# Kernel tuning notes

Hardware: AMD Instinct MI355X
Metric: run time of the kernel (lower is better)

Reference implementation:

```python
import jax, jax.numpy as jnp
import numpy as np

N_NODES = 50000
N_EDGES = 400000
LATENT = 128
HIDDEN = 512
N_HEADS = 2          # latent // 64, NodeAttn default num_heads
HEAD_DIM = LATENT // N_HEADS
N_GRAPHS = 500
LN_EPS = 1e-5


def setup_inputs() -> dict:
    key = jax.random.key(0)
    ks = jax.random.split(key, 24)
    s = 0.02
    inp = {
        "edges": jax.random.randint(ks[0], (2, N_EDGES), 0, N_NODES, dtype=jnp.int32),
        "node_feat": jax.random.normal(ks[1], (N_NODES, LATENT), jnp.float32),
        "edge_attr": jax.random.normal(ks[2], (N_EDGES, LATENT), jnp.float32),
        "u": jax.random.normal(ks[3], (N_GRAPHS, LATENT), jnp.float32),
        "num_nodes": jnp.full((N_GRAPHS,), N_NODES // N_GRAPHS, jnp.int32),
        # NodeAttn params (shared for sent/received calls, as in the module)
        "w1": jax.random.normal(ks[4], (3 * LATENT, LATENT), jnp.float32) * s,
        "b1": jnp.zeros((LATENT,), jnp.float32),
        "w2": jax.random.normal(ks[5], (N_HEADS, HEAD_DIM), jnp.float32) * s,
        "w3": jax.random.normal(ks[6], (2 * LATENT, LATENT), jnp.float32) * s,
        "b3": jnp.zeros((LATENT,), jnp.float32),
        # Encoder MLP: 4*latent -> hidden -> hidden -> latent, LN before ReLU
        "mw0": jax.random.normal(ks[7], (4 * LATENT, HIDDEN), jnp.float32) * s,
        "mb0": jnp.zeros((HIDDEN,), jnp.float32),
        "ls0": jnp.ones((HIDDEN,), jnp.float32),
        "lb0": jnp.zeros((HIDDEN,), jnp.float32),
        "mw1": jax.random.normal(ks[8], (HIDDEN, HIDDEN), jnp.float32) * s,
        "mb1": jnp.zeros((HIDDEN,), jnp.float32),
        "ls1": jnp.ones((HIDDEN,), jnp.float32),
        "lb1": jnp.zeros((HIDDEN,), jnp.float32),
        "mw2": jax.random.normal(ks[9], (HIDDEN, LATENT), jnp.float32) * s,
        "mb2": jnp.zeros((LATENT,), jnp.float32),
    }
    return inp


def _layer_norm(x, scale, bias):
    mu = jnp.mean(x, axis=-1, keepdims=True)
    var = jnp.mean(jnp.square(x - mu), axis=-1, keepdims=True)
    return (x - mu) * jax.lax.rsqrt(var + LN_EPS) * scale + bias


def _node_attn(q, k, ea, index, n_nodes, w1, b1, w2, w3, b3):
    # per-edge multi-head scores -> segment softmax over destination index -> scatter-add
    h = jax.nn.leaky_relu(jnp.concatenate([q, k, ea], axis=-1) @ w1 + b1, 0.2)
    h = h.reshape(-1, N_HEADS, HEAD_DIM)                    # [E, H, D]
    logits = jnp.einsum("ehd,hd->eh", h, w2)                 # [E, H]
    m = jax.ops.segment_max(logits, index, num_segments=n_nodes)
    m = jnp.where(jnp.isfinite(m), m, 0.0)                   # empty segments
    e = jnp.exp(logits - m[index])
    z = jax.ops.segment_sum(e, index, num_segments=n_nodes)
    alpha = e / (z[index] + 1e-16)                           # [E, H]
    v = (jnp.concatenate([k, ea], axis=-1) @ w3 + b3).reshape(-1, N_HEADS, HEAD_DIM)
    out = jax.ops.segment_sum(alpha[..., None] * v, index, num_segments=n_nodes)
    return out.reshape(n_nodes, LATENT)


def reference(edges, node_feat, edge_attr, u, num_nodes, w1, b1, w2, w3, b3,
              mw0, mb0, ls0, lb0, mw1, mb1, ls1, lb1, mw2, mb2):
    n = node_feat.shape[0]
    row, col = edges[0], edges[1]
    sent = _node_attn(node_feat[row], node_feat[col], edge_attr, row, n, w1, b1, w2, w3, b3)
    recv = _node_attn(node_feat[col], node_feat[row], edge_attr, col, n, w1, b1, w2, w3, b3)
    glob = jnp.repeat(u, num_nodes, axis=0, total_repeat_length=n)
    x = jnp.concatenate([node_feat, sent, recv, glob], axis=1)   # [N, 4*latent]
    h = jax.nn.relu(_layer_norm(x @ mw0 + mb0, ls0, lb0))
    h = jax.nn.relu(_layer_norm(h @ mw1 + mb1, ls1, lb1))
    return h @ mw2 + mb2
```

## Files before the change

### kernel.cpp

```cpp
#include <hip/hip_runtime.h>
#include <math.h>

#define LATENT 128

typedef __attribute__((ext_vector_type(8))) short bf16x8;
typedef __attribute__((ext_vector_type(4))) float f32x4;
typedef __attribute__((ext_vector_type(2))) float f32x2;
typedef __attribute__((ext_vector_type(2))) int i32x2;
typedef __attribute__((ext_vector_type(2))) unsigned u32x2;
typedef __attribute__((ext_vector_type(4))) unsigned u32x4;

union U4B { uint4 u; bf16x8 v; };

template <typename T>
__device__ __forceinline__ T ntl(const T* p) { return __builtin_nontemporal_load(p); }

__device__ __forceinline__ unsigned short f2bf(float f) {
    unsigned int x = __float_as_uint(f);
    unsigned int r = (x + 0x7fffu + ((x >> 16) & 1u)) >> 16;
    return (unsigned short)r;
}
__device__ __forceinline__ float bf2f(unsigned short h) {
    return __uint_as_float(((unsigned int)h) << 16);
}
__device__ __forceinline__ unsigned pk2(float a, float b) {
    return (unsigned)f2bf(a) | ((unsigned)f2bf(b) << 16);
}

__device__ __forceinline__ void gld16(const void* g, void* l) {
    __builtin_amdgcn_global_load_lds(
        (const __attribute__((address_space(1))) unsigned int*)g,
        (__attribute__((address_space(3))) unsigned int*)l, 16, 0, 0);
}

__global__ void k_gid(const int* __restrict__ num_nodes, int G, int n, int* __restrict__ gid) {
    __shared__ int goff[1025];
    if (threadIdx.x == 0) {
        int acc = 0;
        for (int g = 0; g < G; ++g) { goff[g] = acc; acc += num_nodes[g]; }
        goff[G] = acc;
    }
    __syncthreads();
    for (int g = 0; g < G; ++g) {
        int s = goff[g];
        int e = goff[g + 1]; if (e > n) e = n;
        for (int i = s + (int)threadIdx.x; i < e; i += blockDim.x) gid[i] = g;
    }
}

#define FN  1152
#define FE3 1248
#define FEV 1280
__global__ __launch_bounds__(256) void k_pack2(const float* __restrict__ mw0,
                                               const float* __restrict__ mw1,
                                               const float* __restrict__ mw2,
                                               const float* __restrict__ w1,
                                               const float* __restrict__ w3,
                                               uint4* __restrict__ pw) {
    int tid = blockIdx.x * 256 + threadIdx.x;
    if (tid >= 1312 * 64) return;
    int fid = tid >> 6, lane = tid & 63;
    const float* src; int kt, nt, N;
    if (fid < 512)       { src = mw0;            kt = fid >> 5;           nt = fid & 31;           N = 512; }
    else if (fid < 1024) { src = mw1;            kt = (fid - 512) >> 5;   nt = (fid - 512) & 31;   N = 512; }
    else if (fid < 1152) { src = mw2;            kt = (fid - 1024) >> 3;  nt = (fid - 1024) & 7;   N = 128; }
    else if (fid < 1184) { src = w1;             kt = (fid - 1152) >> 3;  nt = (fid - 1152) & 7;   N = 128; }
    else if (fid < 1216) { src = w1 + 128 * 128; kt = (fid - 1184) >> 3;  nt = (fid - 1184) & 7;   N = 128; }
    else if (fid < 1248) { src = w3;             kt = (fid - 1216) >> 3;  nt = (fid - 1216) & 7;   N = 128; }
    else if (fid < 1280) { src = w1 + 256 * 128; kt = (fid - 1248) >> 3;  nt = (fid - 1248) & 7;   N = 128; }
    else                 { src = w3 + 128 * 128; kt = (fid - 1280) >> 3;  nt = (fid - 1280) & 7;   N = 128; }
    int col = nt * 16 + (lane & 15);
    int k0 = kt * 32 + (lane >> 4) * 8;
    unsigned int w[4];
#pragma unroll
    for (int p = 0; p < 4; ++p) {
        unsigned int lo = f2bf(src[(size_t)(k0 + 2 * p) * N + col]);
        unsigned int hi = f2bf(src[(size_t)(k0 + 2 * p + 1) * N + col]);
        w[p] = lo | (hi << 16);
    }
    pw[(size_t)fid * 64 + lane] = make_uint4(w[0], w[1], w[2], w[3]);
}

__global__ void k_count(const int* __restrict__ edges, int E,
                        int* __restrict__ deg_s, int* __restrict__ deg_r) {
    int e = blockIdx.x * 256 + threadIdx.x;
    if (e < E) { atomicAdd(&deg_s[edges[e]], 1); atomicAdd(&deg_r[edges[E + e]], 1); }
}

__global__ __launch_bounds__(1024) void k_scan(const int* __restrict__ deg, int n,
                                               int* __restrict__ rowptr, int* __restrict__ cursor) {
    __shared__ int wsum[16];
    int t = threadIdx.x;
    int chunk = (n + 1023) / 1024;
    int s = t * chunk; if (s > n) s = n;
    int epos = s + chunk; if (epos > n) epos = n;
    int sum = 0;
    for (int i = s; i < epos; ++i) sum += deg[i];
    int lane = t & 63, wid = t >> 6;
    int v = sum;
#pragma unroll
    for (int d = 1; d < 64; d <<= 1) { int o = __shfl_up(v, d); if (lane >= d) v += o; }
    if (lane == 63) wsum[wid] = v;
    __syncthreads();
    if (t < 16) {
        int wv = wsum[t];
#pragma unroll
        for (int d = 1; d < 16; d <<= 1) { int o = __shfl_up(wv, d, 16); if (t >= d) wv += o; }
        wsum[t] = wv;
    }
    __syncthreads();
    int woff = wid ? wsum[wid - 1] : 0;
    int run = v + woff - sum;
    for (int i = s; i < epos; ++i) { rowptr[i] = run; cursor[i] = run; run += deg[i]; }
    if (t == 1023) rowptr[n] = run;
}

__global__ void k_fill(const int* __restrict__ edges, int E,
                       int* __restrict__ cur_s, int* __restrict__ cur_r,
                       int* __restrict__ os_s, int* __restrict__ os_r,
                       int* __restrict__ sm_s, int* __restrict__ sm_r) {
    int e = blockIdx.x * 256 + threadIdx.x;
    if (e < E) {
        int r = edges[e], c = edges[E + e];
        int p = atomicAdd(&cur_s[r], 1); os_s[p] = c; sm_s[e] = p;
        int q = atomicAdd(&cur_r[c], 1); os_r[q] = r; sm_r[e] = q;
    }
}

__global__ __launch_bounds__(512) void k_nodepre2(const float* __restrict__ nf, int n,
                                                  const uint4* __restrict__ pw,
                                                  unsigned short* __restrict__ PQK,
                                                  unsigned short* __restrict__ PVh) {
    __shared__ uint4 xs[32 * 64];
    int t = threadIdx.x, lane = t & 63, w = t >> 6;
    int wr = w >> 2, wc = w & 3, l15 = lane & 15, lg = lane >> 4;
    int base = blockIdx.x * 128;
#pragma unroll
    for (int it = 0; it < 4; ++it) {
        int chunk = t + it * 512;
        int row = chunk >> 4, k8 = chunk & 15, k = k8 * 8;
        int node = base + row;
        f32x4 v0 = (f32x4)(0.f), v1 = (f32x4)(0.f);
        if (node < n) {
            const f32x4* s4 = (const f32x4*)(nf + (size_t)node * 128 + k);
            v0 = ntl(s4); v1 = ntl(s4 + 1);
        }
        uint4 pkv;
        pkv.x = pk2(v0.x, v0.y); pkv.y = pk2(v0.z, v0.w);
        pkv.z = pk2(v1.x, v1.y); pkv.w = pk2(v1.z, v1.w);
        int kt = k >> 5, g = (k >> 3) & 3;
        xs[(kt * 8 + (row >> 4)) * 64 + g * 16 + (row & 15)] = pkv;
    }
    __syncthreads();
    f32x4 acc[4][6];
#pragma unroll
    for (int rt = 0; rt < 4; ++rt)
#pragma unroll
        for (int ct = 0; ct < 6; ++ct) acc[rt][ct] = (f32x4)(0.f);
    for (int kt = 0; kt < 4; ++kt) {
        U4B a[4];
#pragma unroll
        for (int rt = 0; rt < 4; ++rt) a[rt].u = xs[(kt * 8 + wr * 4 + rt) * 64 + lane];
        U4B b[6];
#pragma unroll
        for (int ct = 0; ct < 6; ++ct) {
            int nt = wc * 6 + ct;
            int mat = nt >> 3, ntm = nt & 7;
            b[ct].u = pw[(size_t)(FN + mat * 32 + kt * 8 + ntm) * 64 + lane];
        }
#pragma unroll
        for (int rt = 0; rt < 4; ++rt)
#pragma unroll
            for (int ct = 0; ct < 6; ++ct)
                acc[rt][ct] = __builtin_amdgcn_mfma_f32_16x16x32_bf16(a[rt].v, b[ct].v, acc[rt][ct], 0, 0, 0);
    }
#pragma unroll
    for (int rt = 0; rt < 4; ++rt)
#pragma unroll
        for (int ct = 0; ct < 6; ++ct) {
            int nt = wc * 6 + ct;
#pragma unroll
            for (int reg = 0; reg < 4; ++reg) {
                int node = base + (wr * 4 + rt) * 16 + lg * 4 + reg;
                if (node < n) {
                    unsigned short hv = f2bf(acc[rt][ct][reg]);
                    if (nt < 16) PQK[(size_t)node * 256 + nt * 16 + l15] = hv;
                    else         PVh[(size_t)node * 128 + (nt - 16) * 16 + l15] = hv;
                }
            }
        }
}

__global__ __launch_bounds__(256) void k_eproj1(const int* __restrict__ edges,
                                                const float* __restrict__ ea, int E,
                                                const uint4* __restrict__ pw,
                                                const unsigned short* __restrict__ PQK,
                                                const float* __restrict__ b1,
                                                const float* __restrict__ w2,
                                                const int* __restrict__ sm_s,
                                                const int* __restrict__ sm_r,
                                                unsigned short* __restrict__ EVs,
                                                unsigned short* __restrict__ EVr,
                                                float* __restrict__ ess2, float* __restrict__ ers2) {
    __shared__ uint4 xs[16 * 64];
    __shared__ unsigned short edata[64 * 128];
    __shared__ unsigned short evdata[64 * 128];
    int t = threadIdx.x, lane = t & 63, w = t >> 6;
    int wc = w, l15 = lane & 15, lg = lane >> 4;
    int base = blockIdx.x * 64;
#pragma unroll
    for (int it = 0; it < 4; ++it) {
        int chunk = t + it * 256;
        int row = chunk >> 4, k8 = chunk & 15, k = k8 * 8;
        int e = base + row;
        f32x4 v0 = (f32x4)(0.f), v1 = (f32x4)(0.f);
        if (e < E) {
            const f32x4* s4 = (const f32x4*)(ea + (size_t)e * 128 + k);
            v0 = ntl(s4); v1 = ntl(s4 + 1);
        }
        uint4 pkv;
        pkv.x = pk2(v0.x, v0.y); pkv.y = pk2(v0.z, v0.w);
        pkv.z = pk2(v1.x, v1.y); pkv.w = pk2(v1.z, v1.w);
        int kt = k >> 5, g = (k >> 3) & 3;
        xs[(kt * 4 + (row >> 4)) * 64 + g * 16 + (row & 15)] = pkv;
    }
    __syncthreads();
    f32x4 acc[4][4];
#pragma unroll
    for (int rt = 0; rt < 4; ++rt)
#pragma unroll
        for (int ct = 0; ct < 4; ++ct) acc[rt][ct] = (f32x4)(0.f);
    for (int kt = 0; kt < 4; ++kt) {
        U4B a[4];
#pragma unroll
        for (int rt = 0; rt < 4; ++rt) a[rt].u = xs[(kt * 4 + rt) * 64 + lane];
        U4B b[4];
        b[0].u = pw[(size_t)(FE3 + kt * 8 + wc * 2 + 0) * 64 + lane];
        b[1].u = pw[(size_t)(FE3 + kt * 8 + wc * 2 + 1) * 64 + lane];
        b[2].u = pw[(size_t)(FEV + kt * 8 + wc * 2 + 0) * 64 + lane];
        b[3].u = pw[(size_t)(FEV + kt * 8 + wc * 2 + 1) * 64 + lane];
#pragma unroll
        for (int rt = 0; rt < 4; ++rt)
#pragma unroll
            for (int ct = 0; ct < 4; ++ct)
                acc[rt][ct] = __builtin_amdgcn_mfma_f32_16x16x32_bf16(a[rt].v, b[ct].v, acc[rt][ct], 0, 0, 0);
    }
#pragma unroll
    for (int rt = 0; rt < 4; ++rt)
#pragma unroll
        for (int cc = 0; cc < 2; ++cc) {
            int col = (wc * 2 + cc) * 16 + l15;
#pragma unroll
            for (int reg = 0; reg < 4; ++reg) {
                int e_loc = rt * 16 + lg * 4 + reg;
                edata[e_loc * 128 + col]  = f2bf(acc[rt][cc][reg]);
                evdata[e_loc * 128 + col] = f2bf(acc[rt][2 + cc][reg]);
            }
        }
    __syncthreads();
    {
        int e4 = lane >> 4, piece = lane & 15;
#pragma unroll
        for (int i = 0; i < 4; ++i) {
            int e_loc = w * 16 + i * 4 + e4;
            int e = base + e_loc;
            if (e < E) {
                u32x4 v = *(const u32x4*)&evdata[e_loc * 128 + piece * 8];
                __builtin_nontemporal_store(v, (u32x4*)(EVs + (size_t)sm_s[e] * 128 + piece * 8));
                __builtin_nontemporal_store(v, (u32x4*)(EVr + (size_t)sm_r[e] * 128 + piece * 8));
            }
        }
    }
    int esub = lane >> 3, dg = lane & 7;
    float b1r[16], w2r[16];
    {
        const float4* b4 = (const float4*)(b1 + dg * 16);
        const float4* w4 = (const float4*)(w2 + (dg >> 2) * 64 + (dg & 3) * 16);
#pragma unroll
        for (int q = 0; q < 4; ++q) {
            float4 bv = b4[q], wv = w4[q];
            b1r[q * 4 + 0] = bv.x; b1r[q * 4 + 1] = bv.y; b1r[q * 4 + 2] = bv.z; b1r[q * 4 + 3] = bv.w;
            w2r[q * 4 + 0] = wv.x; w2r[q * 4 + 1] = wv.y; w2r[q * 4 + 2] = wv.z; w2r[q * 4 + 3] = wv.w;
        }
    }
#pragma unroll
    for (int it = 0; it < 2; ++it) {
        int e_loc = w * 16 + it * 8 + esub;
        int e = base + e_loc;
        if (e >= E) break;
        int r = edges[e], c = edges[E + e];
        const uint4* Aqr = (const uint4*)(PQK + ((size_t)r << 8) + dg * 16);
        const uint4* Akc = (const uint4*)(PQK + ((size_t)c << 8) + 128 + dg * 16);
        const uint4* Aqc = (const uint4*)(PQK + ((size_t)c << 8) + dg * 16);
        const uint4* Akr = (const uint4*)(PQK + ((size_t)r << 8) + 128 + dg * 16);
        const uint4* Ae3 = (const uint4*)(&edata[e_loc * 128 + dg * 16]);
        float ps = 0.f, pr = 0.f;
#pragma unroll
        for (int half = 0; half < 2; ++half) {
            uint4 uqr = Aqr[half], ukc = Akc[half], uqc = Aqc[half], ukr = Akr[half], ue3 = Ae3[half];
            unsigned wqr[4] = {uqr.x, uqr.y, uqr.z, uqr.w};
            unsigned wkc[4] = {ukc.x, ukc.y, ukc.z, ukc.w};
            unsigned wqc[4] = {uqc.x, uqc.y, uqc.z, uqc.w};
            unsigned wkr[4] = {ukr.x, ukr.y, ukr.z, ukr.w};
            unsigned we3[4] = {ue3.x, ue3.y, ue3.z, ue3.w};
#pragma unroll
            for (int q = 0; q < 4; ++q) {
#pragma unroll
                for (int hl = 0; hl < 2; ++hl) {
                    int i = half * 8 + q * 2 + hl;
                    float fqr = hl ? __uint_as_float(wqr[q] & 0xffff0000u) : __uint_as_float(wqr[q] << 16);
                    float fkc = hl ? __uint_as_float(wkc[q] & 0xffff0000u) : __uint_as_float(wkc[q] << 16);
                    float fqc = hl ? __uint_as_float(wqc[q] & 0xffff0000u) : __uint_as_float(wqc[q] << 16);
                    float fkr = hl ? __uint_as_float(wkr[q] & 0xffff0000u) : __uint_as_float(wkr[q] << 16);
                    float fe3 = hl ? __uint_as_float(we3[q] & 0xffff0000u) : __uint_as_float(we3[q] << 16);
                    float com = fe3 + b1r[i];
                    float hs = fqr + fkc + com; hs = hs > 0.f ? hs : 0.2f * hs;
                    float hr = fqc + fkr + com; hr = hr > 0.f ? hr : 0.2f * hr;
                    ps += hs * w2r[i]; pr += hr * w2r[i];
                }
            }
        }
        ps += __shfl_xor(ps, 1); ps += __shfl_xor(ps, 2);
        pr += __shfl_xor(pr, 1); pr += __shfl_xor(pr, 2);
        float Es = expf(ps), Er = expf(pr);
        if (dg == 0) {
            __builtin_nontemporal_store(Es, &ess2[(size_t)sm_s[e] * 2]);
            __builtin_nontemporal_store(Er, &ers2[(size_t)sm_r[e] * 2]);
        } else if (dg == 4) {
            __builtin_nontemporal_store(Es, &ess2[(size_t)sm_s[e] * 2 + 1]);
            __builtin_nontemporal_store(Er, &ers2[(size_t)sm_r[e] * 2 + 1]);
        }
    }
}

__global__ __launch_bounds__(256) void k_aggr(int n,
                                              const int* __restrict__ rps, const int* __restrict__ os_s,
                                              const int* __restrict__ rpr, const int* __restrict__ os_r,
                                              const float* __restrict__ ess2, const float* __restrict__ ers2,
                                              const unsigned short* __restrict__ PVh,
                                              const unsigned short* __restrict__ EVs,
                                              const unsigned short* __restrict__ EVr,
                                              const float* __restrict__ b3,
                                              unsigned short* __restrict__ out_sh,
                                              unsigned short* __restrict__ out_rh) {
    int w = threadIdx.x >> 6, lane = threadIdx.x & 63;
    int unit = blockIdx.x * 4 + w;
    if (unit >= 2 * n) return;
    bool sent = unit < n;
    int node = sent ? unit : unit - n;
    const int*   rp = sent ? rps : rpr;
    const int*   os = sent ? os_s : os_r;
    const float* ex = sent ? ess2 : ers2;
    const unsigned* EVx = (const unsigned*)(sent ? EVs : EVr);
    const unsigned* PV32 = (const unsigned*)PVh;
    int s0 = rp[node], s1 = rp[node + 1];
    float b3a = b3[2 * lane], b3b = b3[2 * lane + 1];
    float z0 = 0.f, z1 = 0.f, acca = 0.f, accb = 0.f;
    int j = s0;
    for (; j + 4 <= s1; j += 4) {
        int oth[4]; f32x2 ez[4]; unsigned ev[4], pv[4];
#pragma unroll
        for (int q = 0; q < 4; ++q) oth[q] = os[j + q];
#pragma unroll
        for (int q = 0; q < 4; ++q) ez[q] = ntl((const f32x2*)(ex + 2 * (j + q)));
#pragma unroll
        for (int q = 0; q < 4; ++q) ev[q] = ntl(EVx + (size_t)(j + q) * 64 + lane);
#pragma unroll
        for (int q = 0; q < 4; ++q) pv[q] = PV32[(size_t)oth[q] * 64 + lane];
#pragma unroll
        for (int q = 0; q < 4; ++q) {
            float va = __uint_as_float(ev[q] << 16) + __uint_as_float(pv[q] << 16) + b3a;
            float vb = __uint_as_float(ev[q] & 0xffff0000u) + __uint_as_float(pv[q] & 0xffff0000u) + b3b;
            z0 += ez[q].x; z1 += ez[q].y;
            float aw = (lane < 32) ? ez[q].x : ez[q].y;
            acca += aw * va; accb += aw * vb;
        }
    }
    for (; j < s1; ++j) {
        int oth = os[j];
        f32x2 ez = ntl((const f32x2*)(ex + 2 * j));
        unsigned ev = ntl(EVx + (size_t)j * 64 + lane);
        unsigned pv = PV32[(size_t)oth * 64 + lane];
        float va = __uint_as_float(ev << 16) + __uint_as_float(pv << 16) + b3a;
        float vb = __uint_as_float(ev & 0xffff0000u) + __uint_as_float(pv & 0xffff0000u) + b3b;
        z0 += ez.x; z1 += ez.y;
        float aw = (lane < 32) ? ez.x : ez.y;
        acca += aw * va; accb += aw * vb;
    }
    float zz = (lane < 32) ? z0 : z1;
    float rz = 1.f / (zz + 1e-16f);
    unsigned o = pk2(acca * rz, accb * rz);
    unsigned* outp = (unsigned*)(sent ? out_sh : out_rh);
    outp[(size_t)node * 64 + lane] = o;
}

__global__ __launch_bounds__(512, 4) void k_mlp12(
    const float* __restrict__ nf, const unsigned short* __restrict__ out_sh,
    const unsigned short* __restrict__ out_rh,
    const float* __restrict__ u, const int* __restrict__ gid, int n,
    const uint4* __restrict__ pw,
    const float* __restrict__ mb0, const float* __restrict__ ls0, const float* __restrict__ lb0,
    const float* __restrict__ mb1, const float* __restrict__ ls1, const float* __restrict__ lb1,
    const float* __restrict__ mb2, float* __restrict__ out) {
    extern __shared__ char smem[];
    char* hx = smem;
    char* bb = smem + 32768;
    float2* red = (float2*)(smem + 65536);

    int t = threadIdx.x, lane = t & 63, w = t >> 6;
    int wr = w >> 2, wc = w & 3, l15 = lane & 15, lg = lane >> 4;
    int base = blockIdx.x * 32;

    auto stage32 = [&](int fragbase) {
        const uint4* src = pw + (size_t)fragbase * 64;
#pragma unroll
        for (int q = 0; q < 4; ++q)
            gld16(src + q * 512 + t, bb + ((size_t)q * 512 + t) * 16);
    };
    auto stage8 = [&](int fragbase) {
        const uint4* src = pw + (size_t)fragbase * 64;
        gld16(src + t, bb + (size_t)t * 16);
    };

    stage32(0);
#pragma unroll
    for (int it = 0; it < 8; ++it) {
        int chunk = t + it * 512;
        int row = chunk >> 7, kq = chunk & 127;
        int k = kq * 4;
        int node = base + row;
        u32x2 p = (u32x2)(0u);
        if (node < n) {
            int kk = k & 127;
            if (k < 128) {
                f32x4 v = ntl((const f32x4*)(nf + (size_t)node * 128 + kk));
                p.x = pk2(v.x, v.y); p.y = pk2(v.z, v.w);
            } else if (k < 384) {
                const unsigned short* s = (k < 256 ? out_sh : out_rh) + (size_t)node * 128 + kk;
                p = ntl((const u32x2*)s);
            } else {
                f32x4 v = *(const f32x4*)(u + (size_t)gid[node] * 128 + kk);
                p.x = pk2(v.x, v.y); p.y = pk2(v.z, v.w);
            }
        }
        int addr = (row * 1024 + k * 2) ^ ((row & 7) << 4);
        *(u32x2*)(hx + addr) = p;
    }
    __syncthreads();

    f32x4 acc[8];
#pragma unroll
    for (int layer = 0; layer < 2; ++layer) {
        const float* MB = layer ? mb1 : mb0;
        const float* LS = layer ? ls1 : ls0;
        const float* LB = layer ? lb1 : lb0;
        const int fbase = layer ? 512 : 0;
#pragma unroll
        for (int ct = 0; ct < 8; ++ct) acc[ct] = (f32x4)(0.f);

        for (int kt = 0; kt < 16; ++kt) {
            U4B b[8];
#pragma unroll
            for (int ct = 0; ct < 8; ++ct)
                b[ct].u = *(const uint4*)(bb + (((size_t)wc * 8 + ct) * 64 + lane) * 16);
            U4B a;
            {
                int row = wr * 16 + l15;
                int addr = (row * 1024 + kt * 64 + lg * 16) ^ ((row & 7) << 4);
                a.u = *(const uint4*)(hx + addr);
            }
            __syncthreads();
            if (kt < 15)            stage32(fbase + (kt + 1) * 32);
            else if (layer == 0)    stage32(512);
            else                    stage8(1024);
            __builtin_amdgcn_s_setprio(1);
#pragma unroll
            for (int ct = 0; ct < 8; ++ct)
                acc[ct] = __builtin_amdgcn_mfma_f32_16x16x32_bf16(a.v, b[ct].v, acc[ct], 0, 0, 0);
            __builtin_amdgcn_s_setprio(0);
            __syncthreads();
        }

        float mbv[8], lsv[8], lbv[8];
#pragma unroll
        for (int ct = 0; ct < 8; ++ct) {
            int col = wc * 128 + ct * 16 + l15;
            mbv[ct] = MB[col]; lsv[ct] = LS[col]; lbv[ct] = LB[col];
        }
#pragma unroll
        for (int reg = 0; reg < 4; ++reg) {
            float p = 0.f, q = 0.f;
#pragma unroll
            for (int ct = 0; ct < 8; ++ct) {
                float y = acc[ct][reg] + mbv[ct];
                acc[ct][reg] = y;
                p += y; q += y * y;
            }
#pragma unroll
            for (int d = 1; d < 16; d <<= 1) { p += __shfl_xor(p, d); q += __shfl_xor(q, d); }
            if (l15 == 0) {
                int row = wr * 16 + lg * 4 + reg;
                red[row * 4 + wc] = make_float2(p, q);
            }
        }
        __syncthreads();
#pragma unroll
        for (int reg = 0; reg < 4; ++reg) {
            int row = wr * 16 + lg * 4 + reg;
            float2 r0 = red[row * 4 + 0], r1 = red[row * 4 + 1];
            float2 r2 = red[row * 4 + 2], r3 = red[row * 4 + 3];
            float S = r0.x + r1.x + r2.x + r3.x;
            float S2 = r0.y + r1.y + r2.y + r3.y;
            float mu = S * (1.f / 512.f);
            float var = S2 * (1.f / 512.f) - mu * mu;
            float rs = rsqrtf(var + 1e-5f);
            int rswz = (row & 7) << 4;
#pragma unroll
            for (int ct = 0; ct < 8; ++ct) {
                float h = (acc[ct][reg] - mu) * rs * lsv[ct] + lbv[ct];
                h = fmaxf(h, 0.f);
                int col = wc * 128 + ct * 16 + l15;
                int addr = (row * 1024 + col * 2) ^ rswz;
                *(unsigned short*)(hx + addr) = f2bf(h);
            }
        }
        __syncthreads();
    }

    f32x4 a2[2];
#pragma unroll
    for (int ct = 0; ct < 2; ++ct) a2[ct] = (f32x4)(0.f);
    for (int kt = 0; kt < 16; ++kt) {
        U4B b[2];
#pragma unroll
        for (int ct = 0; ct < 2; ++ct)
            b[ct].u = *(const uint4*)(bb + (((size_t)wc * 2 + ct) * 64 + lane) * 16);
        U4B a;
        {
            int row = wr * 16 + l15;
            int addr = (row * 1024 + kt * 64 + lg * 16) ^ ((row & 7) << 4);
            a.u = *(const uint4*)(hx + addr);
        }
        __syncthreads();
        if (kt < 15) stage8(1024 + (kt + 1) * 8);
        __builtin_amdgcn_s_setprio(1);
#pragma unroll
        for (int ct = 0; ct < 2; ++ct)
            a2[ct] = __builtin_amdgcn_mfma_f32_16x16x32_bf16(a.v, b[ct].v, a2[ct], 0, 0, 0);
        __builtin_amdgcn_s_setprio(0);
        __syncthreads();
    }
    float mb2v[2];
#pragma unroll
    for (int ct = 0; ct < 2; ++ct) mb2v[ct] = mb2[wc * 32 + ct * 16 + l15];
#pragma unroll
    for (int reg = 0; reg < 4; ++reg) {
        int node = base + wr * 16 + lg * 4 + reg;
        if (node < n) {
#pragma unroll
            for (int ct = 0; ct < 2; ++ct)
                __builtin_nontemporal_store(a2[ct][reg] + mb2v[ct],
                    &out[(size_t)node * 128 + wc * 32 + ct * 16 + l15]);
        }
    }
}

extern "C" void kernel_launch(void* const* d_in, const int* in_sizes, int n_in,
                              void* d_out, int out_size, void* d_ws, size_t ws_size,
                              hipStream_t stream) {
    const int*   edges     = (const int*)d_in[0];
    const float* nf        = (const float*)d_in[1];
    const float* ea        = (const float*)d_in[2];
    const float* u         = (const float*)d_in[3];
    const int*   num_nodes = (const int*)d_in[4];
    const float* w1  = (const float*)d_in[5];
    const float* b1  = (const float*)d_in[6];
    const float* w2  = (const float*)d_in[7];
    const float* w3  = (const float*)d_in[8];
    const float* b3  = (const float*)d_in[9];
    const float* mw0 = (const float*)d_in[10];
    const float* mb0 = (const float*)d_in[11];
    const float* ls0 = (const float*)d_in[12];
    const float* lb0 = (const float*)d_in[13];
    const float* mw1 = (const float*)d_in[14];
    const float* mb1 = (const float*)d_in[15];
    const float* ls1 = (const float*)d_in[16];
    const float* lb1 = (const float*)d_in[17];
    const float* mw2 = (const float*)d_in[18];
    const float* mb2 = (const float*)d_in[19];

    int E = in_sizes[0] / 2;
    int n = in_sizes[1] / LATENT;
    int G = in_sizes[4];
    float* out = (float*)d_out;

    char* wsb = (char*)d_ws;
    size_t off = 0;
    auto alloc = [&](size_t bytes) { void* p = (void*)(wsb + off); off += (bytes + 15) & ~(size_t)15; return p; };
    uint4*          pw     = (uint4*)alloc((size_t)1312 * 64 * 16);
    unsigned short* PQK    = (unsigned short*)alloc((size_t)n * 256 * 2);
    unsigned short* PVh    = (unsigned short*)alloc((size_t)n * 128 * 2);
    unsigned short* EVs    = (unsigned short*)alloc((size_t)E * 128 * 2);
    unsigned short* EVr    = (unsigned short*)alloc((size_t)E * 128 * 2);
    float*          ess2   = (float*)alloc((size_t)E * 2 * 4);
    float*          ers2   = (float*)alloc((size_t)E * 2 * 4);
    unsigned short* out_sh = (unsigned short*)alloc((size_t)n * 128 * 2);
    unsigned short* out_rh = (unsigned short*)alloc((size_t)n * 128 * 2);
    int*            gid    = (int*)alloc((size_t)n * 4);
    int*            deg_s  = (int*)alloc((size_t)n * 4);
    int*            deg_r  = (int*)alloc((size_t)n * 4);
    int*            cur_s  = (int*)alloc((size_t)n * 4);
    int*            cur_r  = (int*)alloc((size_t)n * 4);
    int*            rps    = (int*)alloc((size_t)(n + 1) * 4);
    int*            rpr    = (int*)alloc((size_t)(n + 1) * 4);
    int*            os_s   = (int*)alloc((size_t)E * 4);
    int*            os_r   = (int*)alloc((size_t)E * 4);
    int*            sm_s   = (int*)alloc((size_t)E * 4);
    int*            sm_r   = (int*)alloc((size_t)E * 4);

    hipMemsetAsync(deg_s, 0, (size_t)2 * n * 4 + 16, stream);

    hipFuncSetAttribute((const void*)k_mlp12, hipFuncAttributeMaxDynamicSharedMemorySize, 66560);

    k_gid<<<1, 256, 0, stream>>>(num_nodes, G, n, gid);
    k_pack2<<<(1312 * 64 + 255) / 256, 256, 0, stream>>>(mw0, mw1, mw2, w1, w3, pw);
    k_count<<<(E + 255) / 256, 256, 0, stream>>>(edges, E, deg_s, deg_r);
    k_scan<<<1, 1024, 0, stream>>>(deg_s, n, rps, cur_s);
    k_scan<<<1, 1024, 0, stream>>>(deg_r, n, rpr, cur_r);
    k_fill<<<(E + 255) / 256, 256, 0, stream>>>(edges, E, cur_s, cur_r, os_s, os_r, sm_s, sm_r);
    k_nodepre2<<<(n + 127) / 128, 512, 0, stream>>>(nf, n, pw, PQK, PVh);
    k_eproj1<<<(E + 63) / 64, 256, 0, stream>>>(edges, ea, E, pw, PQK, b1, w2, sm_s, sm_r,
                                                EVs, EVr, ess2, ers2);
    k_aggr<<<(2 * n + 3) / 4, 256, 0, stream>>>(n, rps, os_s, rpr, os_r,
                                                ess2, ers2, PVh, EVs, EVr, b3, out_sh, out_rh);
    k_mlp12<<<(n + 31) / 32, 512, 66560, stream>>>(nf, out_sh, out_rh, u, gid, n, pw,
                                                   mb0, ls0, lb0, mb1, ls1, lb1, mb2, out);
}
```

Before: 826.4 us.

## Fold node value projection and bias into per-edge values in edge kernel

The edge projection kernel now gathers the node-side value projection (PVh) for both endpoints, adds the edge part and b3, and writes full per-edge value vectors in CSR order for each direction. The aggregation kernel then streams these vectors sequentially instead of gathering PVh through the other-endpoint index arrays, which are removed along with their writes in the fill kernel. This moves the random node gathers from the aggregation kernel into the edge kernel, where each edge does two 256-byte gathers. The sum is rounded to bf16 once more before being stored.

```diff
diff --git a/kernel.cpp b/kernel.cpp
--- a/kernel.cpp
+++ b/kernel.cpp
@@ -6,7 +6,6 @@
 typedef __attribute__((ext_vector_type(8))) short bf16x8;
 typedef __attribute__((ext_vector_type(4))) float f32x4;
 typedef __attribute__((ext_vector_type(2))) float f32x2;
-typedef __attribute__((ext_vector_type(2))) int i32x2;
 typedef __attribute__((ext_vector_type(2))) unsigned u32x2;
 typedef __attribute__((ext_vector_type(4))) unsigned u32x4;
 
@@ -26,6 +25,8 @@
 __device__ __forceinline__ unsigned pk2(float a, float b) {
     return (unsigned)f2bf(a) | ((unsigned)f2bf(b) << 16);
 }
+__device__ __forceinline__ float lo16(unsigned u) { return __uint_as_float(u << 16); }
+__device__ __forceinline__ float hi16(unsigned u) { return __uint_as_float(u & 0xffff0000u); }
 
 __device__ __forceinline__ void gld16(const void* g, void* l) {
     __builtin_amdgcn_global_load_lds(
@@ -117,13 +118,12 @@
 
 __global__ void k_fill(const int* __restrict__ edges, int E,
                        int* __restrict__ cur_s, int* __restrict__ cur_r,
-                       int* __restrict__ os_s, int* __restrict__ os_r,
                        int* __restrict__ sm_s, int* __restrict__ sm_r) {
     int e = blockIdx.x * 256 + threadIdx.x;
     if (e < E) {
         int r = edges[e], c = edges[E + e];
-        int p = atomicAdd(&cur_s[r], 1); os_s[p] = c; sm_s[e] = p;
-        int q = atomicAdd(&cur_r[c], 1); os_r[q] = r; sm_r[e] = q;
+        sm_s[e] = atomicAdd(&cur_s[r], 1);
+        sm_r[e] = atomicAdd(&cur_r[c], 1);
     }
 }
 
@@ -195,12 +195,14 @@
                                                 const float* __restrict__ ea, int E,
                                                 const uint4* __restrict__ pw,
                                                 const unsigned short* __restrict__ PQK,
+                                                const unsigned short* __restrict__ PVh,
                                                 const float* __restrict__ b1,
                                                 const float* __restrict__ w2,
+                                                const float* __restrict__ b3,
                                                 const int* __restrict__ sm_s,
                                                 const int* __restrict__ sm_r,
-                                                unsigned short* __restrict__ EVs,
-                                                unsigned short* __restrict__ EVr,
+                                                unsigned short* __restrict__ Vs,
+                                                unsigned short* __restrict__ Vr,
                                                 float* __restrict__ ess2, float* __restrict__ ers2) {
     __shared__ uint4 xs[16 * 64];
     __shared__ unsigned short edata[64 * 128];
@@ -260,14 +262,28 @@
     __syncthreads();
     {
         int e4 = lane >> 4, piece = lane & 15;
+        f32x4 b3a = *(const f32x4*)(b3 + piece * 8);
+        f32x4 b3b = *(const f32x4*)(b3 + piece * 8 + 4);
+        float b3v[8] = {b3a.x, b3a.y, b3a.z, b3a.w, b3b.x, b3b.y, b3b.z, b3b.w};
 #pragma unroll
         for (int i = 0; i < 4; ++i) {
             int e_loc = w * 16 + i * 4 + e4;
             int e = base + e_loc;
             if (e < E) {
-                u32x4 v = *(const u32x4*)&evdata[e_loc * 128 + piece * 8];
-                __builtin_nontemporal_store(v, (u32x4*)(EVs + (size_t)sm_s[e] * 128 + piece * 8));
-                __builtin_nontemporal_store(v, (u32x4*)(EVr + (size_t)sm_r[e] * 128 + piece * 8));
+                int r = edges[e], c = edges[E + e];
+                u32x4 vev = *(const u32x4*)&evdata[e_loc * 128 + piece * 8];
+                u32x4 pvc = *(const u32x4*)(PVh + (size_t)c * 128 + piece * 8);
+                u32x4 pvr = *(const u32x4*)(PVh + (size_t)r * 128 + piece * 8);
+                u32x4 vs, vr;
+#pragma unroll
+                for (int q = 0; q < 4; ++q) {
+                    float e0 = lo16(vev[q]) + b3v[2 * q];
+                    float e1 = hi16(vev[q]) + b3v[2 * q + 1];
+                    vs[q] = pk2(e0 + lo16(pvc[q]), e1 + hi16(pvc[q]));
+                    vr[q] = pk2(e0 + lo16(pvr[q]), e1 + hi16(pvr[q]));
+                }
+                __builtin_nontemporal_store(vs, (u32x4*)(Vs + (size_t)sm_s[e] * 128 + piece * 8));
+                __builtin_nontemporal_store(vr, (u32x4*)(Vr + (size_t)sm_r[e] * 128 + piece * 8));
             }
         }
     }
@@ -308,11 +324,11 @@
 #pragma unroll
                 for (int hl = 0; hl < 2; ++hl) {
                     int i = half * 8 + q * 2 + hl;
-                    float fqr = hl ? __uint_as_float(wqr[q] & 0xffff0000u) : __uint_as_float(wqr[q] << 16);
-                    float fkc = hl ? __uint_as_float(wkc[q] & 0xffff0000u) : __uint_as_float(wkc[q] << 16);
-                    float fqc = hl ? __uint_as_float(wqc[q] & 0xffff0000u) : __uint_as_float(wqc[q] << 16);
-                    float fkr = hl ? __uint_as_float(wkr[q] & 0xffff0000u) : __uint_as_float(wkr[q] << 16);
-                    float fe3 = hl ? __uint_as_float(we3[q] & 0xffff0000u) : __uint_as_float(we3[q] << 16);
+                    float fqr = hl ? hi16(wqr[q]) : lo16(wqr[q]);
+                    float fkc = hl ? hi16(wkc[q]) : lo16(wkc[q]);
+                    float fqc = hl ? hi16(wqc[q]) : lo16(wqc[q]);
+                    float fkr = hl ? hi16(wkr[q]) : lo16(wkr[q]);
+                    float fe3 = hl ? hi16(we3[q]) : lo16(we3[q]);
                     float com = fe3 + b1r[i];
                     float hs = fqr + fkc + com; hs = hs > 0.f ? hs : 0.2f * hs;
                     float hr = fqc + fkr + com; hr = hr > 0.f ? hr : 0.2f * hr;
@@ -334,13 +350,10 @@
 }
 
 __global__ __launch_bounds__(256) void k_aggr(int n,
-                                              const int* __restrict__ rps, const int* __restrict__ os_s,
-                                              const int* __restrict__ rpr, const int* __restrict__ os_r,
+                                              const int* __restrict__ rps, const int* __restrict__ rpr,
                                               const float* __restrict__ ess2, const float* __restrict__ ers2,
-                                              const unsigned short* __restrict__ PVh,
-                                              const unsigned short* __restrict__ EVs,
-                                              const unsigned short* __restrict__ EVr,
-                                              const float* __restrict__ b3,
+                                              const unsigned short* __restrict__ Vs,
+                                              const unsigned short* __restrict__ Vr,
                                               unsigned short* __restrict__ out_sh,
                                               unsigned short* __restrict__ out_rh) {
     int w = threadIdx.x >> 6, lane = threadIdx.x & 63;
@@ -348,44 +361,31 @@
     if (unit >= 2 * n) return;
     bool sent = unit < n;
     int node = sent ? unit : unit - n;
-    const int*   rp = sent ? rps : rpr;
-    const int*   os = sent ? os_s : os_r;
-    const float* ex = sent ? ess2 : ers2;
-    const unsigned* EVx = (const unsigned*)(sent ? EVs : EVr);
-    const unsigned* PV32 = (const unsigned*)PVh;
+    const int*      rp = sent ? rps : rpr;
+    const float*    ex = sent ? ess2 : ers2;
+    const unsigned* V  = (const unsigned*)(sent ? Vs : Vr);
     int s0 = rp[node], s1 = rp[node + 1];
-    float b3a = b3[2 * lane], b3b = b3[2 * lane + 1];
     float z0 = 0.f, z1 = 0.f, acca = 0.f, accb = 0.f;
     int j = s0;
     for (; j + 4 <= s1; j += 4) {
-        int oth[4]; f32x2 ez[4]; unsigned ev[4], pv[4];
-#pragma unroll
-        for (int q = 0; q < 4; ++q) oth[q] = os[j + q];
+        f32x2 ez[4]; unsigned v[4];
 #pragma unroll
         for (int q = 0; q < 4; ++q) ez[q] = ntl((const f32x2*)(ex + 2 * (j + q)));
 #pragma unroll
-        for (int q = 0; q < 4; ++q) ev[q] = ntl(EVx + (size_t)(j + q) * 64 + lane);
-#pragma unroll
-        for (int q = 0; q < 4; ++q) pv[q] = PV32[(size_t)oth[q] * 64 + lane];
+        for (int q = 0; q < 4; ++q) v[q] = ntl(V + (size_t)(j + q) * 64 + lane);
 #pragma unroll
         for (int q = 0; q < 4; ++q) {
-            float va = __uint_as_float(ev[q] << 16) + __uint_as_float(pv[q] << 16) + b3a;
-            float vb = __uint_as_float(ev[q] & 0xffff0000u) + __uint_as_float(pv[q] & 0xffff0000u) + b3b;
             z0 += ez[q].x; z1 += ez[q].y;
             float aw = (lane < 32) ? ez[q].x : ez[q].y;
-            acca += aw * va; accb += aw * vb;
+            acca += aw * lo16(v[q]); accb += aw * hi16(v[q]);
         }
     }
     for (; j < s1; ++j) {
-        int oth = os[j];
         f32x2 ez = ntl((const f32x2*)(ex + 2 * j));
-        unsigned ev = ntl(EVx + (size_t)j * 64 + lane);
-        unsigned pv = PV32[(size_t)oth * 64 + lane];
-        float va = __uint_as_float(ev << 16) + __uint_as_float(pv << 16) + b3a;
-        float vb = __uint_as_float(ev & 0xffff0000u) + __uint_as_float(pv & 0xffff0000u) + b3b;
+        unsigned v = ntl(V + (size_t)j * 64 + lane);
         z0 += ez.x; z1 += ez.y;
         float aw = (lane < 32) ? ez.x : ez.y;
-        acca += aw * va; accb += aw * vb;
+        acca += aw * lo16(v); accb += aw * hi16(v);
     }
     float zz = (lane < 32) ? z0 : z1;
     float rz = 1.f / (zz + 1e-16f);
@@ -600,8 +600,8 @@
     uint4*          pw     = (uint4*)alloc((size_t)1312 * 64 * 16);
     unsigned short* PQK    = (unsigned short*)alloc((size_t)n * 256 * 2);
     unsigned short* PVh    = (unsigned short*)alloc((size_t)n * 128 * 2);
-    unsigned short* EVs    = (unsigned short*)alloc((size_t)E * 128 * 2);
-    unsigned short* EVr    = (unsigned short*)alloc((size_t)E * 128 * 2);
+    unsigned short* Vs     = (unsigned short*)alloc((size_t)E * 128 * 2);
+    unsigned short* Vr     = (unsigned short*)alloc((size_t)E * 128 * 2);
     float*          ess2   = (float*)alloc((size_t)E * 2 * 4);
     float*          ers2   = (float*)alloc((size_t)E * 2 * 4);
     unsigned short* out_sh = (unsigned short*)alloc((size_t)n * 128 * 2);
@@ -613,8 +613,6 @@
     int*            cur_r  = (int*)alloc((size_t)n * 4);
     int*            rps    = (int*)alloc((size_t)(n + 1) * 4);
     int*            rpr    = (int*)alloc((size_t)(n + 1) * 4);
-    int*            os_s   = (int*)alloc((size_t)E * 4);
-    int*            os_r   = (int*)alloc((size_t)E * 4);
     int*            sm_s   = (int*)alloc((size_t)E * 4);
     int*            sm_r   = (int*)alloc((size_t)E * 4);
 
@@ -627,12 +625,11 @@
     k_count<<<(E + 255) / 256, 256, 0, stream>>>(edges, E, deg_s, deg_r);
     k_scan<<<1, 1024, 0, stream>>>(deg_s, n, rps, cur_s);
     k_scan<<<1, 1024, 0, stream>>>(deg_r, n, rpr, cur_r);
-    k_fill<<<(E + 255) / 256, 256, 0, stream>>>(edges, E, cur_s, cur_r, os_s, os_r, sm_s, sm_r);
+    k_fill<<<(E + 255) / 256, 256, 0, stream>>>(edges, E, cur_s, cur_r, sm_s, sm_r);
     k_nodepre2<<<(n + 127) / 128, 512, 0, stream>>>(nf, n, pw, PQK, PVh);
-    k_eproj1<<<(E + 63) / 64, 256, 0, stream>>>(edges, ea, E, pw, PQK, b1, w2, sm_s, sm_r,
-                                                EVs, EVr, ess2, ers2);
-    k_aggr<<<(2 * n + 3) / 4, 256, 0, stream>>>(n, rps, os_s, rpr, os_r,
-                                                ess2, ers2, PVh, EVs, EVr, b3, out_sh, out_rh);
+    k_eproj1<<<(E + 63) / 64, 256, 0, stream>>>(edges, ea, E, pw, PQK, PVh, b1, w2, b3,
+                                                sm_s, sm_r, Vs, Vr, ess2, ers2);
+    k_aggr<<<(2 * n + 3) / 4, 256, 0, stream>>>(n, rps, rpr, ess2, ers2, Vs, Vr, out_sh, out_rh);
     k_mlp12<<<(n + 31) / 32, 512, 66560, stream>>>(nf, out_sh, out_rh, u, gid, n, pw,
                                                    mb0, ls0, lb0, mb1, ls1, lb1, mb2, out);
 }
```

Measured after the change: 820.8 us. Within noise of the previous version (-0.7%).
